# Optimization experiments

Hardware: AMD Instinct MI355X
Metric: run time of the kernel (lower is better)

The kernel has to match this reference:

```python
import jax, jax.numpy as jnp
import numpy as np

N_NODES = 100000
N_EDGES = 3200000
IN_CH = 35
NUM_FAM = 26
EMBED = 8
NEW_IN = 6 + EMBED + (IN_CH - 6 - NUM_FAM)  # 17
HID = 64
LN_EPS = 1e-5


def setup_inputs() -> dict:
    key = jax.random.key(0)
    ks = jax.random.split(key, 16)
    x = jax.random.normal(ks[0], (N_NODES, IN_CH), dtype=jnp.float32)
    edge_index = jax.random.randint(ks[1], (2, N_EDGES), 0, N_NODES, dtype=jnp.int64)
    s = 0.05
    p = {
        'W_embed': jax.random.normal(ks[2], (NUM_FAM, EMBED), jnp.float32) * s,
        'b_embed': jnp.zeros((EMBED,), jnp.float32),
        'ln_g': jnp.ones((EMBED,), jnp.float32),
        'ln_b': jnp.zeros((EMBED,), jnp.float32),
        'Wl1': jax.random.normal(ks[3], (NEW_IN, HID), jnp.float32) * s,
        'bl1': jnp.zeros((HID,), jnp.float32),
        'Wr1': jax.random.normal(ks[4], (NEW_IN, HID), jnp.float32) * s,
        'Wl2': jax.random.normal(ks[5], (HID, HID), jnp.float32) * s,
        'bl2': jnp.zeros((HID,), jnp.float32),
        'Wr2': jax.random.normal(ks[6], (HID, HID), jnp.float32) * s,
        'Wl3': jax.random.normal(ks[7], (HID, HID), jnp.float32) * s,
        'bl3': jnp.zeros((HID,), jnp.float32),
        'Wr3': jax.random.normal(ks[8], (HID, HID), jnp.float32) * s,
        'Wfc': jax.random.normal(ks[9], (HID, 1), jnp.float32) * s,
        'bfc': jnp.zeros((1,), jnp.float32),
    }
    return {'x': x, 'edge_index': edge_index, **p}


def _sage(h, src, dst, Wl, bl, Wr, n):
    # PyG SAGEConv (mean aggr): lin_l(mean_{j in N(i)} h_j) + lin_r(h_i)
    msum = jax.ops.segment_sum(h[src], dst, num_segments=n)
    cnt = jax.ops.segment_sum(jnp.ones((src.shape[0],), h.dtype), dst, num_segments=n)
    mean = msum / jnp.maximum(cnt, 1.0)[:, None]
    return mean @ Wl + bl + h @ Wr


def reference(x, edge_index, W_embed, b_embed, ln_g, ln_b,
              Wl1, bl1, Wr1, Wl2, bl2, Wr2, Wl3, bl3, Wr3, Wfc, bfc):
    n = x.shape[0]
    src, dst = edge_index[0], edge_index[1]
    node_type = x[:, :6]
    onehot = x[:, 6:6 + NUM_FAM]
    other = x[:, 6 + NUM_FAM:]
    emb = onehot @ W_embed + b_embed
    mu = jnp.mean(emb, axis=-1, keepdims=True)
    var = jnp.var(emb, axis=-1, keepdims=True)
    emb = (emb - mu) * jax.lax.rsqrt(var + LN_EPS) * ln_g + ln_b
    h0 = jnp.concatenate([node_type, emb, other], axis=1)  # [N, 17]
    h1 = jax.nn.relu(_sage(h0, src, dst, Wl1, bl1, Wr1, n))
    h2 = jax.nn.relu(_sage(h1, src, dst, Wl2, bl2, Wr2, n) + h1)
    h3 = jax.nn.relu(_sage(h2, src, dst, Wl3, bl3, Wr3, n) + h2)
    return (h3 @ Wfc + bfc).squeeze(-1)
```

## Files before the change

kernel.cpp:

```cpp
#include <hip/hip_runtime.h>

#define NN 100000
#define NE 3200000
#define NB1 196
#define BCAP2 17664
#define EPB 4096
#define NPB 782

typedef _Float16 half8 __attribute__((ext_vector_type(8)));
typedef float    f32x4 __attribute__((ext_vector_type(4)));

__global__ __launch_bounds__(256) void k_h0(const float* __restrict__ x,
    const float* __restrict__ We, const float* __restrict__ be,
    const float* __restrict__ lg, const float* __restrict__ lb,
    _Float16* __restrict__ h0p)
{
  __shared__ float xs[256 * 35];
  int tid = threadIdx.x;
  int base_node = blockIdx.x * 256;
  int nvalid = NN - base_node; if (nvalid > 256) nvalid = 256;
  int total = nvalid * 35;
  const float* srcp = x + (size_t)base_node * 35;
  for (int j = tid; j < total; j += 256) xs[j] = srcp[j];
  __syncthreads();
  int i = base_node + tid;
  if (i >= NN) return;
  const float* xr = xs + tid * 35;
  float e[8];
  #pragma unroll
  for (int j = 0; j < 8; ++j) e[j] = be[j];
  #pragma unroll
  for (int k = 0; k < 26; ++k) {
    float o = xr[6 + k];
    #pragma unroll
    for (int j = 0; j < 8; ++j) e[j] = fmaf(o, We[k * 8 + j], e[j]);
  }
  float mu = 0.f;
  #pragma unroll
  for (int j = 0; j < 8; ++j) mu += e[j];
  mu *= 0.125f;
  float var = 0.f;
  #pragma unroll
  for (int j = 0; j < 8; ++j) { float d = e[j] - mu; var = fmaf(d, d, var); }
  var *= 0.125f;
  float rs = rsqrtf(var + 1e-5f);

  _Float16 row[32];
  #pragma unroll
  for (int j = 0; j < 6; ++j) row[j] = (_Float16)xr[j];
  #pragma unroll
  for (int j = 0; j < 8; ++j) row[6 + j] = (_Float16)((e[j] - mu) * rs * lg[j] + lb[j]);
  #pragma unroll
  for (int j = 0; j < 3; ++j) row[14 + j] = (_Float16)xr[32 + j];
  #pragma unroll
  for (int j = 17; j < 32; ++j) row[j] = (_Float16)0.f;
  half8* dst = (half8*)(h0p + (size_t)i * 32);
  #pragma unroll
  for (int q = 0; q < 4; ++q) dst[q] = *(half8*)(row + q * 8);
}

__global__ __launch_bounds__(256) void k_partA(const int* __restrict__ ei,
    int* __restrict__ gcur, int* __restrict__ ebuf)
{
  __shared__ int hist[NB1];
  __shared__ int lofs[NB1];
  __shared__ int gb[NB1];
  __shared__ int cur[NB1];
  __shared__ int sd[256];
  __shared__ int stage[EPB];
  __shared__ unsigned char sbkt[EPB];
  int tid = threadIdx.x;
  int base = blockIdx.x * EPB;
  int n = NE - base; if (n > EPB) n = EPB;
  if (tid < NB1) hist[tid] = 0;
  __syncthreads();
  int s[16], d[16];
  #pragma unroll
  for (int k = 0; k < 16; ++k) {
    int idx = tid + k * 256;
    if (idx < n) {
      s[k] = ei[base + idx];
      d[k] = ei[NE + base + idx];
      atomicAdd(&hist[d[k] >> 9], 1);
    } else { s[k] = -1; d[k] = 0; }
  }
  __syncthreads();
  int v = (tid < NB1) ? hist[tid] : 0;
  sd[tid] = v; __syncthreads();
  for (int off = 1; off < 256; off <<= 1) {
    int t = (tid >= off) ? sd[tid - off] : 0;
    __syncthreads(); sd[tid] += t; __syncthreads();
  }
  int excl = sd[tid] - v;
  if (tid < NB1) {
    lofs[tid] = excl; cur[tid] = excl;
    if (v) gb[tid] = tid * BCAP2 + atomicAdd(&gcur[tid], v);
  }
  __syncthreads();
  #pragma unroll
  for (int k = 0; k < 16; ++k) {
    if (s[k] >= 0) {
      int b = d[k] >> 9;
      int p = atomicAdd(&cur[b], 1);
      stage[p] = (s[k] << 9) | (d[k] & 511);
      sbkt[p] = (unsigned char)b;
    }
  }
  __syncthreads();
  for (int p = tid; p < n; p += 256) {
    int b = sbkt[p];
    int pos = gb[b] + (p - lofs[b]);
    if (pos < (b + 1) * BCAP2) ebuf[pos] = stage[p];
  }
}

__global__ __launch_bounds__(512) void k_partB(const int* __restrict__ gcur,
    const int* __restrict__ ebuf, int2* __restrict__ rowinfo, int* __restrict__ srcs)
{
  __shared__ int lcnt[512];
  __shared__ int sd[512];
  int b = blockIdx.x, tid = threadIdx.x;
  int n = gcur[b]; if (n > BCAP2) n = BCAP2;
  const int* eb = ebuf + (size_t)b * BCAP2;
  lcnt[tid] = 0;
  __syncthreads();
  for (int e = tid; e < n; e += 512) atomicAdd(&lcnt[eb[e] & 511], 1);
  __syncthreads();
  int v = lcnt[tid];
  sd[tid] = v; __syncthreads();
  for (int off = 1; off < 512; off <<= 1) {
    int t = (tid >= off) ? sd[tid - off] : 0;
    __syncthreads(); sd[tid] += t; __syncthreads();
  }
  int excl = sd[tid] - v;
  int node = b * 512 + tid;
  if (node < NN) rowinfo[node] = make_int2(b * BCAP2 + excl, v);
  __syncthreads();
  lcnt[tid] = excl;
  __syncthreads();
  for (int e = tid; e < n; e += 512) {
    int w = eb[e];
    int p = atomicAdd(&lcnt[w & 511], 1);
    srcs[(size_t)b * BCAP2 + p] = w >> 9;
  }
}

template <int W>
__global__ __launch_bounds__(256) void k_agg(const _Float16* __restrict__ hin,
    const int2* __restrict__ rowinfo, const int* __restrict__ srcs,
    _Float16* __restrict__ meanout)
{
  constexpr int GL = W / 8;
  constexpr int NG = 64 / GL;
  int wid = (blockIdx.x * 256 + threadIdx.x) >> 6;
  int lane = threadIdx.x & 63;
  if (wid >= NN) return;
  int i = __builtin_amdgcn_readfirstlane(wid);
  int2 ri = rowinfo[i];
  int rs = ri.x, m = ri.y;
  int g = lane / GL;
  int f = lane % GL;
  const int* __restrict__ sp = srcs + rs;

  float acc[8];
  #pragma unroll
  for (int q = 0; q < 8; ++q) acc[q] = 0.f;

  #pragma unroll 4
  for (int e = g; e < m; e += NG) {
    int src = sp[e];
    half8 v = *(const half8*)(hin + (size_t)src * W + f * 8);
    #pragma unroll
    for (int q = 0; q < 8; ++q) acc[q] += (float)v[q];
  }
  #pragma unroll
  for (int q = 0; q < 8; ++q) {
    #pragma unroll
    for (int off = GL; off < 64; off <<= 1) acc[q] += __shfl_xor(acc[q], off);
  }
  float cm = fmaxf((float)m, 1.f);
  if (lane < GL) {
    _Float16 o[8];
    #pragma unroll
    for (int q = 0; q < 8; ++q) o[q] = (_Float16)(acc[q] / cm);
    *(half8*)(meanout + (size_t)i * W + lane * 8) = *(half8*)o;
  }
}

template <int W, int KW, bool RES, bool FINAL>
__global__ __launch_bounds__(256) void k_mlp(const _Float16* __restrict__ mean,
    const _Float16* __restrict__ h,
    const float* __restrict__ Wl, const float* __restrict__ bl,
    const float* __restrict__ Wr,
    const float* __restrict__ Wfc, const float* __restrict__ bfc,
    void* __restrict__ outp)
{
  __shared__ _Float16 lwl[64 * W];
  __shared__ _Float16 lwr[64 * W];
  int tid = threadIdx.x;
  for (int idx = tid; idx < 64 * W; idx += 256) {
    int nn = idx / W, kk = idx % W;
    lwl[idx] = (kk < KW) ? (_Float16)Wl[kk * 64 + nn] : (_Float16)0.f;
    lwr[idx] = (kk < KW) ? (_Float16)Wr[kk * 64 + nn] : (_Float16)0.f;
  }
  __syncthreads();
  constexpr int NKB = W / 32;
  int wv = tid >> 6, lane = tid & 63;
  int c = lane & 15, kg = lane >> 4;

  half8 bwl[4][NKB], bwr[4][NKB];
  #pragma unroll
  for (int nt = 0; nt < 4; ++nt)
    #pragma unroll
    for (int kb = 0; kb < NKB; ++kb) {
      bwl[nt][kb] = *(const half8*)&lwl[(nt * 16 + c) * W + kb * 32 + kg * 8];
      bwr[nt][kb] = *(const half8*)&lwr[(nt * 16 + c) * W + kb * 32 + kg * 8];
    }

  int wavebase = blockIdx.x * 256 + wv * 64;
  #pragma unroll
  for (int ti = 0; ti < 4; ++ti) {
    int tbase = wavebase + ti * 16;
    if (tbase >= NN) break;
    half8 am[NKB], ah[NKB];
    #pragma unroll
    for (int kb = 0; kb < NKB; ++kb) {
      am[kb] = *(const half8*)(mean + (size_t)(tbase + c) * W + kb * 32 + kg * 8);
      ah[kb] = *(const half8*)(h    + (size_t)(tbase + c) * W + kb * 32 + kg * 8);
    }
    f32x4 acc[4] = {f32x4{0,0,0,0}, f32x4{0,0,0,0}, f32x4{0,0,0,0}, f32x4{0,0,0,0}};
    #pragma unroll
    for (int nt = 0; nt < 4; ++nt)
      #pragma unroll
      for (int kb = 0; kb < NKB; ++kb) {
        acc[nt] = __builtin_amdgcn_mfma_f32_16x16x32_f16(am[kb], bwl[nt][kb], acc[nt], 0, 0, 0);
        acc[nt] = __builtin_amdgcn_mfma_f32_16x16x32_f16(ah[kb], bwr[nt][kb], acc[nt], 0, 0, 0);
      }
    if (!FINAL) {
      _Float16* hout = (_Float16*)outp;
      #pragma unroll
      for (int nt = 0; nt < 4; ++nt) {
        float bia = bl[nt * 16 + c];
        #pragma unroll
        for (int r = 0; r < 4; ++r) {
          int node = tbase + kg * 4 + r;
          float v = acc[nt][r] + bia;
          if (RES) v += (float)h[(size_t)node * 64 + nt * 16 + c];
          hout[(size_t)node * 64 + nt * 16 + c] = (_Float16)fmaxf(v, 0.f);
        }
      }
    } else {
      #pragma unroll
      for (int r = 0; r < 4; ++r) {
        float p = 0.f;
        #pragma unroll
        for (int nt = 0; nt < 4; ++nt) {
          float v = acc[nt][r] + bl[nt * 16 + c];
          if (RES) v += (float)h[(size_t)(tbase + kg * 4 + r) * 64 + nt * 16 + c];
          v = fmaxf(v, 0.f);
          p = fmaf(v, Wfc[nt * 16 + c], p);
        }
        p += __shfl_xor(p, 1); p += __shfl_xor(p, 2);
        p += __shfl_xor(p, 4); p += __shfl_xor(p, 8);
        if (c == 0) ((float*)outp)[tbase + kg * 4 + r] = p + bfc[0];
      }
    }
  }
}

extern "C" void kernel_launch(void* const* d_in, const int* in_sizes, int n_in,
                              void* d_out, int out_size, void* d_ws, size_t ws_size,
                              hipStream_t stream)
{
  const float* x   = (const float*)d_in[0];
  const int*   ei  = (const int*)d_in[1];
  const float* We  = (const float*)d_in[2];
  const float* be  = (const float*)d_in[3];
  const float* lg  = (const float*)d_in[4];
  const float* lb  = (const float*)d_in[5];
  const float* Wl1 = (const float*)d_in[6];
  const float* bl1 = (const float*)d_in[7];
  const float* Wr1 = (const float*)d_in[8];
  const float* Wl2 = (const float*)d_in[9];
  const float* bl2 = (const float*)d_in[10];
  const float* Wr2 = (const float*)d_in[11];
  const float* Wl3 = (const float*)d_in[12];
  const float* bl3 = (const float*)d_in[13];
  const float* Wr3 = (const float*)d_in[14];
  const float* Wfc = (const float*)d_in[15];
  const float* bfc = (const float*)d_in[16];
  (void)in_sizes; (void)n_in; (void)out_size; (void)ws_size;

  size_t off = 0;
  auto carve = [&](size_t bytes) -> void* {
    void* p = (char*)d_ws + off;
    off += (bytes + 255) & ~(size_t)255;
    return p;
  };
  _Float16* h0p    = (_Float16*)carve((size_t)NN * 32 * 2);
  _Float16* mean1  = (_Float16*)carve((size_t)NN * 32 * 2);
  char*     uni    = (char*)carve((size_t)NB1 * BCAP2 * 4);
  int*      ebuf   = (int*)uni;
  _Float16* h1     = (_Float16*)uni;
  _Float16* mean23 = (_Float16*)carve((size_t)NN * 64 * 2);
  _Float16* h2     = (_Float16*)carve((size_t)NN * 64 * 2);
  int*      srcs   = (int*)carve((size_t)NB1 * BCAP2 * 4);
  int2*     rowinfo= (int2*)carve((size_t)NN * 8);
  int*      gcur   = (int*)carve((size_t)NB1 * 4);

  const int nblk_node = (NN + 255) / 256;
  const int nblk_wave = (NN + 3) / 4;

  hipMemsetAsync(gcur, 0, (size_t)NB1 * 4, stream);
  k_h0<<<nblk_node, 256, 0, stream>>>(x, We, be, lg, lb, h0p);
  k_partA<<<NPB, 256, 0, stream>>>(ei, gcur, ebuf);
  k_partB<<<NB1, 512, 0, stream>>>(gcur, ebuf, rowinfo, srcs);

  k_agg<32><<<nblk_wave, 256, 0, stream>>>(h0p, rowinfo, srcs, mean1);
  k_mlp<32, 17, false, false><<<nblk_node, 256, 0, stream>>>(mean1, h0p, Wl1, bl1, Wr1, nullptr, nullptr, h1);
  k_agg<64><<<nblk_wave, 256, 0, stream>>>(h1, rowinfo, srcs, mean23);
  k_mlp<64, 64, true, false><<<nblk_node, 256, 0, stream>>>(mean23, h1, Wl2, bl2, Wr2, nullptr, nullptr, h2);
  k_agg<64><<<nblk_wave, 256, 0, stream>>>(h2, rowinfo, srcs, mean23);
  k_mlp<64, 64, true, true><<<nblk_node, 256, 0, stream>>>(mean23, h2, Wl3, bl3, Wr3, Wfc, bfc, d_out);
}
```

Measured before the change: 369.9 us.

## Map several nodes per wave in aggregation and halve partition bucket width

The mean-aggregation kernel now gives each lane group its own destination node and walks all of that node's edges sequentially, instead of spreading one node's edges across the whole wave. This removes the cross-lane shuffle reduction and the per-node wave overhead, and launches fewer blocks. In exchange, lanes within a wave can diverge when neighbouring nodes have different degrees. The edge partitioning also moves from 512-node buckets to 256-node buckets (391 buckets with smaller capacity), which changes the bucket index width and the scan in both partition kernels.

```diff
diff --git a/kernel.cpp b/kernel.cpp
--- a/kernel.cpp
+++ b/kernel.cpp
@@ -2,8 +2,8 @@
 
 #define NN 100000
 #define NE 3200000
-#define NB1 196
-#define BCAP2 17664
+#define NBK 391
+#define BCAP2 9216
 #define EPB 4096
 #define NPB 782
 
@@ -62,17 +62,17 @@
 __global__ __launch_bounds__(256) void k_partA(const int* __restrict__ ei,
     int* __restrict__ gcur, int* __restrict__ ebuf)
 {
-  __shared__ int hist[NB1];
-  __shared__ int lofs[NB1];
-  __shared__ int gb[NB1];
-  __shared__ int cur[NB1];
+  __shared__ int hist[NBK];
+  __shared__ int lofs[NBK];
+  __shared__ int gb[NBK];
+  __shared__ int cur[NBK];
   __shared__ int sd[256];
   __shared__ int stage[EPB];
-  __shared__ unsigned char sbkt[EPB];
+  __shared__ unsigned short sbkt[EPB];
   int tid = threadIdx.x;
   int base = blockIdx.x * EPB;
   int n = NE - base; if (n > EPB) n = EPB;
-  if (tid < NB1) hist[tid] = 0;
+  for (int b = tid; b < NBK; b += 256) hist[b] = 0;
   __syncthreads();
   int s[16], d[16];
   #pragma unroll
@@ -81,29 +81,30 @@
     if (idx < n) {
       s[k] = ei[base + idx];
       d[k] = ei[NE + base + idx];
-      atomicAdd(&hist[d[k] >> 9], 1);
+      atomicAdd(&hist[d[k] >> 8], 1);
     } else { s[k] = -1; d[k] = 0; }
   }
   __syncthreads();
-  int v = (tid < NB1) ? hist[tid] : 0;
-  sd[tid] = v; __syncthreads();
+  int b0 = 2 * tid, b1 = 2 * tid + 1;
+  int c0 = (b0 < NBK) ? hist[b0] : 0;
+  int c1 = (b1 < NBK) ? hist[b1] : 0;
+  int ls = c0 + c1;
+  sd[tid] = ls; __syncthreads();
   for (int off = 1; off < 256; off <<= 1) {
     int t = (tid >= off) ? sd[tid - off] : 0;
     __syncthreads(); sd[tid] += t; __syncthreads();
   }
-  int excl = sd[tid] - v;
-  if (tid < NB1) {
-    lofs[tid] = excl; cur[tid] = excl;
-    if (v) gb[tid] = tid * BCAP2 + atomicAdd(&gcur[tid], v);
-  }
+  int excl = sd[tid] - ls;
+  if (b0 < NBK) { lofs[b0] = excl;      cur[b0] = excl;      if (c0) gb[b0] = b0 * BCAP2 + atomicAdd(&gcur[b0], c0); }
+  if (b1 < NBK) { lofs[b1] = excl + c0; cur[b1] = excl + c0; if (c1) gb[b1] = b1 * BCAP2 + atomicAdd(&gcur[b1], c1); }
   __syncthreads();
   #pragma unroll
   for (int k = 0; k < 16; ++k) {
     if (s[k] >= 0) {
-      int b = d[k] >> 9;
+      int b = d[k] >> 8;
       int p = atomicAdd(&cur[b], 1);
-      stage[p] = (s[k] << 9) | (d[k] & 511);
-      sbkt[p] = (unsigned char)b;
+      stage[p] = (s[k] << 8) | (d[k] & 255);
+      sbkt[p] = (unsigned short)b;
     }
   }
   __syncthreads();
@@ -117,31 +118,35 @@
 __global__ __launch_bounds__(512) void k_partB(const int* __restrict__ gcur,
     const int* __restrict__ ebuf, int2* __restrict__ rowinfo, int* __restrict__ srcs)
 {
-  __shared__ int lcnt[512];
-  __shared__ int sd[512];
+  __shared__ int lcnt[256];
+  __shared__ int sd[256];
   int b = blockIdx.x, tid = threadIdx.x;
   int n = gcur[b]; if (n > BCAP2) n = BCAP2;
   const int* eb = ebuf + (size_t)b * BCAP2;
-  lcnt[tid] = 0;
-  __syncthreads();
-  for (int e = tid; e < n; e += 512) atomicAdd(&lcnt[eb[e] & 511], 1);
-  __syncthreads();
-  int v = lcnt[tid];
-  sd[tid] = v; __syncthreads();
-  for (int off = 1; off < 512; off <<= 1) {
-    int t = (tid >= off) ? sd[tid - off] : 0;
-    __syncthreads(); sd[tid] += t; __syncthreads();
-  }
-  int excl = sd[tid] - v;
-  int node = b * 512 + tid;
-  if (node < NN) rowinfo[node] = make_int2(b * BCAP2 + excl, v);
-  __syncthreads();
-  lcnt[tid] = excl;
+  if (tid < 256) lcnt[tid] = 0;
+  __syncthreads();
+  for (int e = tid; e < n; e += 512) atomicAdd(&lcnt[eb[e] & 255], 1);
+  __syncthreads();
+  int v = 0;
+  if (tid < 256) { v = lcnt[tid]; sd[tid] = v; }
+  __syncthreads();
+  for (int off = 1; off < 256; off <<= 1) {
+    int t = (tid < 256 && tid >= off) ? sd[tid - off] : 0;
+    __syncthreads();
+    if (tid < 256) sd[tid] += t;
+    __syncthreads();
+  }
+  if (tid < 256) {
+    int excl = sd[tid] - v;
+    int node = b * 256 + tid;
+    if (node < NN) rowinfo[node] = make_int2(b * BCAP2 + excl, v);
+    lcnt[tid] = excl;
+  }
   __syncthreads();
   for (int e = tid; e < n; e += 512) {
     int w = eb[e];
-    int p = atomicAdd(&lcnt[w & 511], 1);
-    srcs[(size_t)b * BCAP2 + p] = w >> 9;
+    int p = atomicAdd(&lcnt[w & 255], 1);
+    srcs[(size_t)b * BCAP2 + p] = w >> 8;
   }
 }
 
@@ -151,15 +156,16 @@
     _Float16* __restrict__ meanout)
 {
   constexpr int GL = W / 8;
-  constexpr int NG = 64 / GL;
-  int wid = (blockIdx.x * 256 + threadIdx.x) >> 6;
+  constexpr int NPW = 64 / GL;
+  int wave = (blockIdx.x * 256 + threadIdx.x) >> 6;
   int lane = threadIdx.x & 63;
-  if (wid >= NN) return;
-  int i = __builtin_amdgcn_readfirstlane(wid);
-  int2 ri = rowinfo[i];
-  int rs = ri.x, m = ri.y;
+  if (wave * NPW >= NN) return;
   int g = lane / GL;
   int f = lane % GL;
+  int node = wave * NPW + g;
+  bool valid = node < NN;
+  int2 ri = valid ? rowinfo[node] : make_int2(0, 0);
+  int rs = ri.x, m = ri.y;
   const int* __restrict__ sp = srcs + rs;
 
   float acc[8];
@@ -167,23 +173,18 @@
   for (int q = 0; q < 8; ++q) acc[q] = 0.f;
 
   #pragma unroll 4
-  for (int e = g; e < m; e += NG) {
-    int src = sp[e];
-    half8 v = *(const half8*)(hin + (size_t)src * W + f * 8);
+  for (int e = 0; e < m; ++e) {
+    half8 v = *(const half8*)(hin + (size_t)sp[e] * W + f * 8);
     #pragma unroll
     for (int q = 0; q < 8; ++q) acc[q] += (float)v[q];
   }
-  #pragma unroll
-  for (int q = 0; q < 8; ++q) {
-    #pragma unroll
-    for (int off = GL; off < 64; off <<= 1) acc[q] += __shfl_xor(acc[q], off);
-  }
-  float cm = fmaxf((float)m, 1.f);
-  if (lane < GL) {
+
+  if (valid) {
+    float r = 1.f / fmaxf((float)m, 1.f);
     _Float16 o[8];
     #pragma unroll
-    for (int q = 0; q < 8; ++q) o[q] = (_Float16)(acc[q] / cm);
-    *(half8*)(meanout + (size_t)i * W + lane * 8) = *(half8*)o;
+    for (int q = 0; q < 8; ++q) o[q] = (_Float16)(acc[q] * r);
+    *(half8*)(meanout + (size_t)node * W + f * 8) = *(half8*)o;
   }
 }
 
@@ -299,27 +300,28 @@
   };
   _Float16* h0p    = (_Float16*)carve((size_t)NN * 32 * 2);
   _Float16* mean1  = (_Float16*)carve((size_t)NN * 32 * 2);
-  char*     uni    = (char*)carve((size_t)NB1 * BCAP2 * 4);
+  char*     uni    = (char*)carve((size_t)NBK * BCAP2 * 4);
   int*      ebuf   = (int*)uni;
   _Float16* h1     = (_Float16*)uni;
   _Float16* mean23 = (_Float16*)carve((size_t)NN * 64 * 2);
   _Float16* h2     = (_Float16*)carve((size_t)NN * 64 * 2);
-  int*      srcs   = (int*)carve((size_t)NB1 * BCAP2 * 4);
+  int*      srcs   = (int*)carve((size_t)NBK * BCAP2 * 4);
   int2*     rowinfo= (int2*)carve((size_t)NN * 8);
-  int*      gcur   = (int*)carve((size_t)NB1 * 4);
-
-  const int nblk_node = (NN + 255) / 256;
-  const int nblk_wave = (NN + 3) / 4;
-
-  hipMemsetAsync(gcur, 0, (size_t)NB1 * 4, stream);
+  int*      gcur   = (int*)carve((size_t)NBK * 4);
+
+  const int nblk_node  = (NN + 255) / 256;
+  const int nblk_agg64 = ((NN + 7) / 8 + 3) / 4;
+  const int nblk_agg32 = ((NN + 15) / 16 + 3) / 4;
+
+  hipMemsetAsync(gcur, 0, (size_t)NBK * 4, stream);
   k_h0<<<nblk_node, 256, 0, stream>>>(x, We, be, lg, lb, h0p);
   k_partA<<<NPB, 256, 0, stream>>>(ei, gcur, ebuf);
-  k_partB<<<NB1, 512, 0, stream>>>(gcur, ebuf, rowinfo, srcs);
-
-  k_agg<32><<<nblk_wave, 256, 0, stream>>>(h0p, rowinfo, srcs, mean1);
+  k_partB<<<NBK, 512, 0, stream>>>(gcur, ebuf, rowinfo, srcs);
+
+  k_agg<32><<<nblk_agg32, 256, 0, stream>>>(h0p, rowinfo, srcs, mean1);
   k_mlp<32, 17, false, false><<<nblk_node, 256, 0, stream>>>(mean1, h0p, Wl1, bl1, Wr1, nullptr, nullptr, h1);
-  k_agg<64><<<nblk_wave, 256, 0, stream>>>(h1, rowinfo, srcs, mean23);
+  k_agg<64><<<nblk_agg64, 256, 0, stream>>>(h1, rowinfo, srcs, mean23);
   k_mlp<64, 64, true, false><<<nblk_node, 256, 0, stream>>>(mean23, h1, Wl2, bl2, Wr2, nullptr, nullptr, h2);
-  k_agg<64><<<nblk_wave, 256, 0, stream>>>(h2, rowinfo, srcs, mean23);
+  k_agg<64><<<nblk_agg64, 256, 0, stream>>>(h2, rowinfo, srcs, mean23);
   k_mlp<64, 64, true, true><<<nblk_node, 256, 0, stream>>>(mean23, h2, Wl3, bl3, Wr3, Wfc, bfc, d_out);
 }
```

After: 371.6 us. No clear change (+0.5%).
